# Performance work log

Measured on AMD Instinct MI355X. Metric: run time of the kernel, lower is better.

The kernel has to match this reference:

```python
import jax, jax.numpy as jnp
import numpy as np
from jax.scipy.linalg import expm
jax.config.update("jax_enable_x64", True)

HBAR = 0.6582119569
CM2EV = 0.00012398419
N6A, N10A = 4, 4
DT = 1.0
KDC = dict(E_S1=3.995, E_S2=4.9183, om6a=596.0 * CM2EV, om10a=919.0 * CM2EV,
           kap6a_S1=-0.0964, kap6a_S2=0.1193, lam=0.1825, gamma=-0.018)


def _build():
    cd = np.complex128

    def ladder(n):
        a = np.zeros((n, n), dtype=cd)
        for k in range(1, n):
            a[k - 1, k] = np.sqrt(float(k))
        adag = a.conj().T
        return (a + adag) / np.sqrt(2.0), adag @ a, np.eye(n, dtype=cd)

    Q6a1, N6a1, I6a = ladder(N6A)
    Q10a1, N10a1, I10a = ladder(N10A)
    Nel, Dvib = 3, N6A * N10A
    Ivib = np.eye(Dvib, dtype=cd)
    Iel = np.eye(Nel, dtype=cd)
    lift = lambda op: np.kron(Iel, op)
    Q6a = lift(np.kron(Q6a1, I10a))
    Q10a = lift(np.kron(I6a, Q10a1))
    N6a = lift(np.kron(N6a1, I10a))
    N10a = lift(np.kron(I6a, N10a1))
    P = []
    for k in range(Nel):
        ek = np.zeros(Nel, dtype=cd); ek[k] = 1.0
        P.append(np.kron(np.outer(ek, ek), Ivib))
    e1 = np.zeros(Nel, dtype=cd); e1[1] = 1.0
    e2 = np.zeros(Nel, dtype=cd); e2[2] = 1.0
    Poff = np.kron(np.outer(e1, e2) + np.outer(e2, e1), Ivib)
    Lj = np.kron(np.outer(e1, e2), Ivib)  # |S1><S2| lift
    D = Nel * Dvib
    I = np.eye(D, dtype=cd)
    p = KDC
    H = (p['E_S1'] * P[1] + p['E_S2'] * P[2] + p['om6a'] * N6a + p['om10a'] * N10a
         + p['kap6a_S1'] * P[1] @ Q6a + p['kap6a_S2'] * P[2] @ Q6a
         + p['lam'] * Poff @ Q10a + p['gamma'] * Poff @ (Q10a @ Q10a))
    # Coherent part -i(I kron H - H^T* kron I); dissipator at unit rate (scaled by g later)
    Lc = -1j * (np.kron(I, H) - np.kron(H.conj().T, I))
    LdL = Lj.conj().T @ Lj
    Ld0 = (np.kron(Lj.conj(), Lj) - 0.5 * np.kron(I, LdL)
           - 0.5 * np.kron(LdL.conj().T, I))
    psi = np.zeros(D, dtype=cd); psi[2 * N6A * N10A] = 1.0
    rho0 = np.outer(psi, psi.conj()).reshape(-1)
    trP = np.stack([P[k].T.reshape(-1) for k in range(3)])  # [3, D^2]
    return Lc, Ld0, rho0, trP

_LC, _LD0, _RHO0, _TRP = _build()


def setup_inputs() -> dict:
    return {"log_g": jnp.asarray(np.log(1.0 / 40.0), dtype=jnp.float32),
            "n_steps": 1000}


def reference(log_g, n_steps):
    Lc = jnp.asarray(_LC)
    Ld0 = jnp.asarray(_LD0)
    rho0 = jnp.asarray(_RHO0)
    trP = jnp.asarray(_TRP)
    g = jnp.exp(log_g).astype(jnp.float64)
    Lsup = Lc + g * Ld0                      # [D^2, D^2] complex128
    U = expm(Lsup * (DT / HBAR))             # one-step propagator

    def step(rho, _):
        pops = jnp.real(trP @ rho)           # tr(P_k rho), k=0..2
        return U @ rho, pops

    _, ps = jax.lax.scan(step, rho0, None, length=int(n_steps))  # [n_steps, 3]
    return (ps[:, 0].astype(jnp.float32),
            ps[:, 1].astype(jnp.float32),
            ps[:, 2].astype(jnp.float32))
```

## Files before the change

### kernel.cpp

```cpp
#include <hip/hip_runtime.h>
#include <math.h>


#define DS 1024
#define MATD ((size_t)DS * DS * sizeof(double))
#define PA 66

typedef double v4d __attribute__((ext_vector_type(4)));

__device__ inline double Qel(int i, int j) {
    if (i == j + 1) return sqrt((double)i) * 0.70710678118654752440;
    if (j == i + 1) return sqrt((double)j) * 0.70710678118654752440;
    return 0.0;
}

__device__ inline void fill_H(double* Hs, int tid) {
    const double CM2EV = 0.00012398419;
    const double E_S1 = 3.995, E_S2 = 4.9183;
    const double om6a = 596.0 * CM2EV, om10a = 919.0 * CM2EV;
    const double kapA = -0.0964, kapB = 0.1193, lam = 0.1825, gam = -0.018;
    for (int h = tid; h < 1024; h += 256) {
        int r = h >> 5, c = h & 31;
        int e = r >> 4, v6 = (r >> 2) & 3, v10 = r & 3;
        int e2 = c >> 4, w6 = (c >> 2) & 3, w10 = c & 3;
        double val = 0.0;
        if (r == c) val += (e ? E_S2 : E_S1) + om6a * v6 + om10a * v10;
        if (e == e2 && v10 == w10) val += (e ? kapB : kapA) * Qel(v6, w6);
        if (e != e2 && v6 == w6) {
            double q2 = 0.0;
            #pragma unroll
            for (int m = 0; m < 4; ++m) q2 += Qel(v10, m) * Qel(m, w10);
            val += lam * Qel(v10, w10) + gam * q2;
        }
        Hs[h] = val;
    }
}

__global__ __launch_bounds__(256)
void build_G10(const float* __restrict__ logg, double* __restrict__ X,
               double* __restrict__ Y, double* __restrict__ Z)
{
    int tid = threadIdx.x;
    if (blockIdx.x >= 4096) {
        int idx = (blockIdx.x - 4096) * 256 + tid;
        if (idx < 64 * 1024) {
            int r = idx >> 10, i = idx & 1023;
            double v = 0.0;
            if (r < 2 && i % 33 == 0) {
                int a = i / 33;
                if ((a < 16) == (r == 0)) v = 1.0;
            }
            Y[idx] = v;
        } else if (idx < 64 * 1024 + 1024) {
            int i = idx - 64 * 1024;
            Z[i] = (i == 528) ? 1.0 : 0.0;
        }
        return;
    }
    __shared__ double Hs[1024];
    fill_H(Hs, tid);
    __syncthreads();
    double g = exp((double)logg[0]);
    const double sc = ((1.0 / 0.6582119569) / 16.0) / 10.0;
    int idx = blockIdx.x * 256 + tid;
    int r = idx >> 10, c = idx & 1023;
    int i = r >> 5, j = r & 31;
    int k = c >> 5, l = c & 31;
    double t = 0.0;
    if (k <= l) {
        if (i <= j) {
            if (i < 16 && j < 16) {
                int p = i + 16, q = j + 16;
                if ((p == k && q == l) || (p == l && q == k)) t += g;
            }
            if (i == k && j == l) t -= 0.5 * g * ((i >= 16) + (j >= 16));
        } else {
            if (j == l) t += Hs[i * 32 + k];
            if (k != l && j == k) t += Hs[i * 32 + l];
            if (i == k) t -= Hs[l * 32 + j];
            if (k != l && i == l) t -= Hs[k * 32 + j];
        }
    } else {
        if (i <= j) {
            double ha = 0.0;
            if (j == l) ha += Hs[i * 32 + k];
            if (j == k) ha -= Hs[i * 32 + l];
            if (i == k) ha -= Hs[l * 32 + j];
            if (i == l) ha += Hs[k * 32 + j];
            t -= ha;
        } else {
            if (i < 16 && j < 16 && (i + 16 == k) && (j + 16 == l)) t += g;
            if (i == k && j == l) t -= 0.5 * g * ((i >= 16) + (j >= 16));
        }
    }
    X[idx] = t * sc + ((r == c) ? 1.0 : 0.0);
}

__global__ __launch_bounds__(256)
void apply_T(const float* __restrict__ logg, const double* __restrict__ M,
             double* __restrict__ O, double invk)
{
    __shared__ double Hs[1024];
    __shared__ int    qlist[112];
    __shared__ double wl[4][112];
    __shared__ int    counts[4];
    __shared__ int    Kshared;
    const int tid = threadIdx.x;
    fill_H(Hs, tid);
    __syncthreads();
    const double g = exp((double)logg[0]);
    const double sck = ((1.0 / 0.6582119569) / 16.0) * invk;

    const int a = blockIdx.x >> 4, b = blockIdx.x & 15;
    const int i0 = a << 1, j0 = b << 1;
    const int wv = tid >> 6, lane = tid & 63;
    const int m = lane & 31;

    bool valid = false; int q = 0;
    double w0 = 0.0, w1 = 0.0, w2 = 0.0, w3 = 0.0;

    if (a != b) {
        if (lane < 32) {
            const bool fam2 = (wv >= 2);
            const int sel = wv & 1;
            if (!fam2) {
                const int js = j0 + sel;
                double cA = Hs[i0 * 32 + m];
                double cB = Hs[(i0 + 1) * 32 + m];
                if (a < b) {
                    if ((cA != 0.0 || cB != 0.0) && m != js) {
                        valid = true;
                        q = (m > js) ? m * 32 + js : js * 32 + m;
                        double sA = (m > js) ? -cA : cA;
                        double sB = (m > js) ? -cB : cB;
                        if (sel == 0) { w0 = sA; w2 = sB; }
                        else          { w1 = sA; w3 = sB; }
                    }
                } else {
                    if (cA != 0.0 || cB != 0.0) {
                        valid = true;
                        q = (m < js) ? m * 32 + js : js * 32 + m;
                        if (sel == 0) { w0 = cA; w2 = cB; }
                        else          { w1 = cA; w3 = cB; }
                    }
                }
            } else {
                const int is = i0 + sel;
                double c0 = Hs[m * 32 + j0];
                double c1 = Hs[m * 32 + j0 + 1];
                if (a < b) {
                    if ((c0 != 0.0 || c1 != 0.0) && m != is) {
                        valid = true;
                        q = (is > m) ? is * 32 + m : m * 32 + is;
                        double s0 = (is > m) ? c0 : -c0;
                        double s1 = (is > m) ? c1 : -c1;
                        if (sel == 0) { w0 = s0; w1 = s1; }
                        else          { w2 = s0; w3 = s1; }
                    }
                } else {
                    if (c0 != 0.0 || c1 != 0.0) {
                        valid = true;
                        q = (m < is) ? m * 32 + is : is * 32 + m;
                        if (sel == 0) { w0 = -c0; w1 = -c1; }
                        else          { w2 = -c0; w3 = -c1; }
                    }
                }
            }
        }
    } else {
        const int ia = i0 + (wv >> 1), ja = j0 + (wv & 1);
        const bool up = (ia <= ja);
        double wr = 0.0;
        if (lane < 32) {
            double c = Hs[ia * 32 + m];
            if (up) {
                if (c != 0.0 && m != ja) {
                    valid = true;
                    q = (m > ja) ? m * 32 + ja : ja * 32 + m;
                    wr = (m > ja) ? -c : c;
                }
            } else {
                if (c != 0.0) {
                    valid = true;
                    q = (m < ja) ? m * 32 + ja : ja * 32 + m;
                    wr = c;
                }
            }
        } else {
            double c = Hs[m * 32 + ja];
            if (up) {
                if (c != 0.0 && m != ia) {
                    valid = true;
                    q = (ia > m) ? ia * 32 + m : m * 32 + ia;
                    wr = (ia > m) ? c : -c;
                }
            } else {
                if (c != 0.0) {
                    valid = true;
                    q = (m < ia) ? m * 32 + ia : ia * 32 + m;
                    wr = -c;
                }
            }
        }
        if (wv == 0) w0 = wr; else if (wv == 1) w1 = wr;
        else if (wv == 2) w2 = wr; else w3 = wr;
    }

    unsigned long long mask = __ballot(valid);
    if (lane == 0) counts[wv] = __popcll(mask);
    __syncthreads();
    int base = 0;
    for (int t = 0; t < wv; ++t) base += counts[t];
    if (valid) {
        int slot = base + __popcll(mask & ((1ull << lane) - 1ull));
        qlist[slot] = q;
        wl[0][slot] = w0; wl[1][slot] = w1; wl[2][slot] = w2; wl[3][slot] = w3;
    }
    __syncthreads();
    if (tid == 0) {
        int K = counts[0] + counts[1] + counts[2] + counts[3];
        const int cnt = (a >= 8) + (b >= 8);
        if (a < 8 && b < 8) {
            #pragma unroll
            for (int r = 0; r < 4; ++r) {
                int ia = i0 + (r >> 1), ja = j0 + (r & 1);
                qlist[K] = (ia + 16) * 32 + (ja + 16);
                wl[0][K] = 0.0; wl[1][K] = 0.0; wl[2][K] = 0.0; wl[3][K] = 0.0;
                wl[r][K] = g; ++K;
            }
        }
        if (cnt > 0) {
            double wd = -0.5 * g * (double)cnt;
            #pragma unroll
            for (int r = 0; r < 4; ++r) {
                int ia = i0 + (r >> 1), ja = j0 + (r & 1);
                qlist[K] = ia * 32 + ja;
                wl[0][K] = 0.0; wl[1][K] = 0.0; wl[2][K] = 0.0; wl[3][K] = 0.0;
                wl[r][K] = wd; ++K;
            }
        }
        while (K & 1) {
            qlist[K] = 0;
            wl[0][K] = 0.0; wl[1][K] = 0.0; wl[2][K] = 0.0; wl[3][K] = 0.0;
            ++K;
        }
        Kshared = K;
    }
    __syncthreads();
    const int K = Kshared;

    double acc[4][4];
    #pragma unroll
    for (int r = 0; r < 4; ++r)
        #pragma unroll
        for (int u = 0; u < 4; ++u) acc[r][u] = 0.0;

    const double2* Mp = (const double2*)M;
    const int e2 = tid << 1;
    for (int k = 0; k < K; k += 2) {
        #pragma unroll
        for (int u = 0; u < 2; ++u) {
            int qq = qlist[k + u];
            double W0 = wl[0][k + u], W1 = wl[1][k + u];
            double W2 = wl[2][k + u], W3 = wl[3][k + u];
            double2 v0 = Mp[(size_t)qq * (DS / 2) + e2];
            double2 v1 = Mp[(size_t)qq * (DS / 2) + e2 + 1];
            acc[0][0] += W0 * v0.x; acc[0][1] += W0 * v0.y;
            acc[0][2] += W0 * v1.x; acc[0][3] += W0 * v1.y;
            acc[1][0] += W1 * v0.x; acc[1][1] += W1 * v0.y;
            acc[1][2] += W1 * v1.x; acc[1][3] += W1 * v1.y;
            acc[2][0] += W2 * v0.x; acc[2][1] += W2 * v0.y;
            acc[2][2] += W2 * v1.x; acc[2][3] += W2 * v1.y;
            acc[3][0] += W3 * v0.x; acc[3][1] += W3 * v0.y;
            acc[3][2] += W3 * v1.x; acc[3][3] += W3 * v1.y;
        }
    }

    const int c0 = tid << 2;
    #pragma unroll
    for (int r = 0; r < 4; ++r) {
        int pr = (i0 + (r >> 1)) * 32 + (j0 + (r & 1));
        size_t bse = (size_t)pr * DS + c0;
        O[bse + 0] = sck * acc[r][0] + ((pr == c0)     ? 1.0 : 0.0);
        O[bse + 1] = sck * acc[r][1] + ((pr == c0 + 1) ? 1.0 : 0.0);
        O[bse + 2] = sck * acc[r][2] + ((pr == c0 + 2) ? 1.0 : 0.0);
        O[bse + 3] = sck * acc[r][3] + ((pr == c0 + 3) ? 1.0 : 0.0);
    }
}

__global__ __launch_bounds__(1024, 1)
void dgemm(const double* __restrict__ A, const double* __restrict__ B,
           double* __restrict__ D)
{
    __shared__ double As[2][64 * PA];
    __shared__ double Bs[2][64 * PA];
    const int tid = threadIdx.x;
    const int bm = blockIdx.x << 6, bn = blockIdx.y << 6;
    const int w = tid >> 6, lane = tid & 63;
    const int lr = lane & 15, lk = lane >> 4;
    const int p = w & 3, kg = w >> 2;
    const int wr = (p >> 1) << 5, wc = (p & 1) << 5;

    v4d acc[2][2];
    #pragma unroll
    for (int si = 0; si < 2; ++si)
        #pragma unroll
        for (int sj = 0; sj < 2; ++sj) acc[si][sj] = (v4d){0., 0., 0., 0.};

    const int ra = tid >> 4;
    const int cs = (tid & 15) << 2;
    const double* gA = A + (size_t)(bm + ra) * DS + cs;
    const double* gB = B + (size_t)ra * DS + bn + cs;
    double va[4], vb[4];
    #pragma unroll
    for (int u = 0; u < 4; ++u) { va[u] = gA[u]; vb[u] = gB[u]; }
    #pragma unroll
    for (int u = 0; u < 4; ++u) {
        As[0][ra * PA + cs + u] = va[u];
        Bs[0][ra * PA + cs + u] = vb[u];
    }
    #pragma unroll
    for (int u = 0; u < 4; ++u) {
        va[u] = gA[64 + u];
        vb[u] = gB[(size_t)64 * DS + u];
    }
    __syncthreads();

    #pragma unroll 2
    for (int kt = 0; kt < DS; kt += 64) {
        const int pb = (kt >> 6) & 1;
        const bool more  = (kt + 64) < DS;
        const bool more2 = (kt + 128) < DS;
        const int k0 = (kg << 4) + lk;
        double A00 = As[pb][(wr + lr) * PA + k0];
        double A10 = As[pb][(wr + 16 + lr) * PA + k0];
        double B00 = Bs[pb][k0 * PA + wc + lr];
        double B10 = Bs[pb][k0 * PA + wc + 16 + lr];
        double A01 = As[pb][(wr + lr) * PA + k0 + 4];
        double A11 = As[pb][(wr + 16 + lr) * PA + k0 + 4];
        double B01 = Bs[pb][(k0 + 4) * PA + wc + lr];
        double B11 = Bs[pb][(k0 + 4) * PA + wc + 16 + lr];
        acc[0][0] = __builtin_amdgcn_mfma_f64_16x16x4f64(A00, B00, acc[0][0], 0, 0, 0);
        acc[0][1] = __builtin_amdgcn_mfma_f64_16x16x4f64(A00, B10, acc[0][1], 0, 0, 0);
        acc[1][0] = __builtin_amdgcn_mfma_f64_16x16x4f64(A10, B00, acc[1][0], 0, 0, 0);
        acc[1][1] = __builtin_amdgcn_mfma_f64_16x16x4f64(A10, B10, acc[1][1], 0, 0, 0);
        acc[0][0] = __builtin_amdgcn_mfma_f64_16x16x4f64(A01, B01, acc[0][0], 0, 0, 0);
        acc[0][1] = __builtin_amdgcn_mfma_f64_16x16x4f64(A01, B11, acc[0][1], 0, 0, 0);
        acc[1][0] = __builtin_amdgcn_mfma_f64_16x16x4f64(A11, B01, acc[1][0], 0, 0, 0);
        acc[1][1] = __builtin_amdgcn_mfma_f64_16x16x4f64(A11, B11, acc[1][1], 0, 0, 0);
        if (more) {
            #pragma unroll
            for (int u = 0; u < 4; ++u) {
                As[pb ^ 1][ra * PA + cs + u] = va[u];
                Bs[pb ^ 1][ra * PA + cs + u] = vb[u];
            }
        }
        if (more2) {
            #pragma unroll
            for (int u = 0; u < 4; ++u) {
                va[u] = gA[kt + 128 + u];
                vb[u] = gB[(size_t)(kt + 128) * DS + u];
            }
        }
        double A02 = As[pb][(wr + lr) * PA + k0 + 8];
        double A12 = As[pb][(wr + 16 + lr) * PA + k0 + 8];
        double B02 = Bs[pb][(k0 + 8) * PA + wc + lr];
        double B12 = Bs[pb][(k0 + 8) * PA + wc + 16 + lr];
        double A03 = As[pb][(wr + lr) * PA + k0 + 12];
        double A13 = As[pb][(wr + 16 + lr) * PA + k0 + 12];
        double B03 = Bs[pb][(k0 + 12) * PA + wc + lr];
        double B13 = Bs[pb][(k0 + 12) * PA + wc + 16 + lr];
        acc[0][0] = __builtin_amdgcn_mfma_f64_16x16x4f64(A02, B02, acc[0][0], 0, 0, 0);
        acc[0][1] = __builtin_amdgcn_mfma_f64_16x16x4f64(A02, B12, acc[0][1], 0, 0, 0);
        acc[1][0] = __builtin_amdgcn_mfma_f64_16x16x4f64(A12, B02, acc[1][0], 0, 0, 0);
        acc[1][1] = __builtin_amdgcn_mfma_f64_16x16x4f64(A12, B12, acc[1][1], 0, 0, 0);
        acc[0][0] = __builtin_amdgcn_mfma_f64_16x16x4f64(A03, B03, acc[0][0], 0, 0, 0);
        acc[0][1] = __builtin_amdgcn_mfma_f64_16x16x4f64(A03, B13, acc[0][1], 0, 0, 0);
        acc[1][0] = __builtin_amdgcn_mfma_f64_16x16x4f64(A13, B03, acc[1][0], 0, 0, 0);
        acc[1][1] = __builtin_amdgcn_mfma_f64_16x16x4f64(A13, B13, acc[1][1], 0, 0, 0);
        __syncthreads();
    }

    double* red = &As[0][0];
    if (kg == 3) {
        #pragma unroll
        for (int si = 0; si < 2; ++si)
            #pragma unroll
            for (int sj = 0; sj < 2; ++sj)
                #pragma unroll
                for (int r = 0; r < 4; ++r)
                    red[(wr + si * 16 + lk + 4 * r) * 64 + wc + sj * 16 + lr]
                        = acc[si][sj][r];
    }
    __syncthreads();
    if (kg == 2) {
        #pragma unroll
        for (int si = 0; si < 2; ++si)
            #pragma unroll
            for (int sj = 0; sj < 2; ++sj)
                #pragma unroll
                for (int r = 0; r < 4; ++r)
                    red[(wr + si * 16 + lk + 4 * r) * 64 + wc + sj * 16 + lr]
                        += acc[si][sj][r];
    }
    __syncthreads();
    if (kg == 1) {
        #pragma unroll
        for (int si = 0; si < 2; ++si)
            #pragma unroll
            for (int sj = 0; sj < 2; ++sj)
                #pragma unroll
                for (int r = 0; r < 4; ++r)
                    red[(wr + si * 16 + lk + 4 * r) * 64 + wc + sj * 16 + lr]
                        += acc[si][sj][r];
    }
    __syncthreads();
    if (kg == 0) {
        #pragma unroll
        for (int si = 0; si < 2; ++si)
            #pragma unroll
            for (int sj = 0; sj < 2; ++sj) {
                int col = bn + wc + sj * 16 + lr;
                #pragma unroll
                for (int r = 0; r < 4; ++r) {
                    int row = bm + wr + si * 16 + lk + 4 * r;
                    D[(size_t)row * DS + col] = acc[si][sj][r]
                        + red[(wr + si * 16 + lk + 4 * r) * 64 + wc + sj * 16 + lr];
                }
            }
    }
}

__global__ __launch_bounds__(256)
void ypart(const double* __restrict__ P, const double* __restrict__ Y,
           double* __restrict__ scratch, int SR)
{
    __shared__ double Yld[32 * 64];
    __shared__ double red[32 * 64];
    const int tid = threadIdx.x;
    const int cc = tid & 63, kw = tid >> 6;
    const int col = (blockIdx.x << 6) + cc;
    const int r0 = blockIdx.z << 5;

    double acc[32];
    #pragma unroll
    for (int r = 0; r < 32; ++r) acc[r] = 0.0;

    for (int kt = 0; kt < 4; ++kt) {
        const int kb = ((blockIdx.y << 2) + kt) << 6;
        __syncthreads();
        for (int idx = tid; idx < 32 * 64; idx += 256) {
            int r = idx >> 6, kk = idx & 63;
            Yld[idx] = Y[(size_t)(r0 + r) * DS + kb + kk];
        }
        __syncthreads();
        #pragma unroll
        for (int kk = 0; kk < 16; ++kk) {
            int kl = (kw << 4) + kk;
            double pv = P[(size_t)(kb + kl) * DS + col];
            #pragma unroll
            for (int r = 0; r < 32; ++r)
                acc[r] += Yld[(r << 6) + kl] * pv;
        }
    }

    __syncthreads();
    if (kw == 3) {
        #pragma unroll
        for (int r = 0; r < 32; ++r) red[(r << 6) + cc] = acc[r];
    }
    __syncthreads();
    if (kw == 2) {
        #pragma unroll
        for (int r = 0; r < 32; ++r) red[(r << 6) + cc] += acc[r];
    }
    __syncthreads();
    if (kw == 1) {
        #pragma unroll
        for (int r = 0; r < 32; ++r) red[(r << 6) + cc] += acc[r];
    }
    __syncthreads();
    if (kw == 0) {
        #pragma unroll
        for (int r = 0; r < 32; ++r) red[(r << 6) + cc] += acc[r];
    }
    __syncthreads();
    for (int idx = tid; idx < 32 * 64; idx += 256) {
        int r = idx >> 6, c2 = idx & 63;
        scratch[((size_t)blockIdx.y * SR + r0 + r) * DS + (blockIdx.x << 6) + c2]
            = red[idx];
    }
}

__global__ __launch_bounds__(256)
void yreduce(const double* __restrict__ scratch, double* __restrict__ Y,
             int M, int SR)
{
    int idx = blockIdx.x * 256 + threadIdx.x;
    int r = idx >> 10, c = idx & 1023;
    double s = 0.0;
    #pragma unroll
    for (int q = 0; q < 4; ++q)
        s += scratch[((size_t)q * SR + r) * DS + c];
    Y[(size_t)(M + r) * DS + c] = s;
}

__global__ __launch_bounds__(256)
void zstep(const double* __restrict__ V, const double* __restrict__ Zin,
           double* __restrict__ Zout)
{
    int row = blockIdx.x * 4 + (threadIdx.x >> 6);
    int lane = threadIdx.x & 63;
    const double2* r_ = (const double2*)(V + (size_t)row * DS);
    const double2* z_ = (const double2*)Zin;
    double s = 0.0;
    #pragma unroll
    for (int k = 0; k < 8; ++k) {
        double2 a = r_[(k << 6) + lane];
        double2 b = z_[(k << 6) + lane];
        s += a.x * b.x + a.y * b.y;
    }
    #pragma unroll
    for (int off = 32; off; off >>= 1) s += __shfl_down(s, off);
    if (lane == 0) Zout[row] = s;
}

__global__ __launch_bounds__(128)
void final_pops(const double* __restrict__ Y, const double* __restrict__ Z,
                float* __restrict__ out, int n)
{
    int t = blockIdx.x;
    int k = threadIdx.x >> 6, lane = threadIdx.x & 63;
    int a = t & 31, j = t >> 5;
    const double* y = Y + (size_t)(2 * a + k) * 1024;
    const double* z = Z + (size_t)j * 1024;
    double s = 0.0;
    for (int i = lane; i < 1024; i += 64) s += y[i] * z[i];
    #pragma unroll
    for (int off = 32; off; off >>= 1) s += __shfl_down(s, off);
    if (lane == 0) {
        out[(size_t)(k + 1) * n + t] = (float)s;
        if (k == 0) out[t] = 0.0f;
    }
}

static inline void ydouble2(const double* P, double* Y, double* scr, int M,
                            hipStream_t stream)
{
    int gz = (M + 31) / 32; if (gz < 1) gz = 1;
    int SR = gz * 32;
    ypart<<<dim3(16, 4, gz), 256, 0, stream>>>(P, Y, scr, SR);
    yreduce<<<SR * 4, 256, 0, stream>>>(scr, Y, M, SR);
}

extern "C" void kernel_launch(void* const* d_in, const int* in_sizes, int n_in,
                              void* d_out, int out_size, void* d_ws, size_t ws_size,
                              hipStream_t stream)
{
    const float* logg = (const float*)d_in[0];
    float* out = (float*)d_out;
    const int n = out_size / 3;
    (void)in_sizes; (void)n_in; (void)ws_size;

    char* ws = (char*)d_ws;
    double* b0 = (double*)(ws + 0 * MATD);
    double* b1 = (double*)(ws + 1 * MATD);
    double* b2 = (double*)(ws + 2 * MATD);
    double* scr = (double*)(ws + 3 * MATD);
    double* Y  = (double*)(ws + 5 * MATD);
    double* Z  = Y + 64 * 1024;

    dim3 g2(16, 16);

    build_G10<<<4096 + 260, 256, 0, stream>>>(logg, b0, Y, Z);
    double* src = b0; double* dst = b1;
    for (int k = 9; k >= 1; --k) {
        apply_T<<<256, 256, 0, stream>>>(logg, src, dst, 1.0 / (double)k);
        double* t = src; src = dst; dst = t;
    }

    dgemm<<<g2, 1024, 0, stream>>>(b1, b1, b0);
    dgemm<<<g2, 1024, 0, stream>>>(b0, b0, b2);
    dgemm<<<g2, 1024, 0, stream>>>(b2, b2, b1);
    dgemm<<<g2, 1024, 0, stream>>>(b1, b1, b0);
    ydouble2(b0, Y, scr, 2, stream);
    dgemm<<<g2, 1024, 0, stream>>>(b0, b0, b1);
    ydouble2(b1, Y, scr, 4, stream);
    dgemm<<<g2, 1024, 0, stream>>>(b1, b1, b2);
    ydouble2(b2, Y, scr, 8, stream);
    dgemm<<<g2, 1024, 0, stream>>>(b2, b2, b1);
    ydouble2(b1, Y, scr, 16, stream);
    dgemm<<<g2, 1024, 0, stream>>>(b1, b1, b2);
    ydouble2(b2, Y, scr, 32, stream);
    dgemm<<<g2, 1024, 0, stream>>>(b2, b2, b1);

    for (int j = 1; j < 32; ++j)
        zstep<<<256, 256, 0, stream>>>(b1, Z + (size_t)(j - 1) * 1024,
                                       Z + (size_t)j * 1024);

    final_pops<<<n, 128, 0, stream>>>(Y, Z, out, n);
}
```

Measured before the change: 763.1 us.

## Split apply_T and ypart work across more blocks for higher parallelism

apply_T now launches 1024 blocks, each handling a quarter of the columns with one element per thread, and uses a swizzled block index so the same row group is spread across XCDs. Its inner loop is unrolled by 8, with the nonzero list padded to a multiple of 8. ypart is split over 16 K-chunks instead of 4 looping ones, and yreduce now sums 16 partials. The aim is to fill the GPU better in these small kernels, at the cost of redundant per-block H setup and more scratch traffic in the reduction.

```diff
diff --git a/kernel.cpp b/kernel.cpp
--- a/kernel.cpp
+++ b/kernel.cpp
@@ -101,8 +101,8 @@
              double* __restrict__ O, double invk)
 {
     __shared__ double Hs[1024];
-    __shared__ int    qlist[112];
-    __shared__ double wl[4][112];
+    __shared__ int    qlist[120];
+    __shared__ double wl[4][120];
     __shared__ int    counts[4];
     __shared__ int    Kshared;
     const int tid = threadIdx.x;
@@ -111,7 +111,9 @@
     const double g = exp((double)logg[0]);
     const double sck = ((1.0 / 0.6582119569) / 16.0) * invk;
 
-    const int a = blockIdx.x >> 4, b = blockIdx.x & 15;
+    const int sw = ((blockIdx.x & 7) << 7) | (blockIdx.x >> 3);
+    const int grp = sw >> 2, q4 = sw & 3;
+    const int a = grp >> 4, b = grp & 15;
     const int i0 = a << 1, j0 = b << 1;
     const int wv = tid >> 6, lane = tid & 63;
     const int m = lane & 31;
@@ -239,7 +241,7 @@
                 wl[r][K] = wd; ++K;
             }
         }
-        while (K & 1) {
+        while (K & 7) {
             qlist[K] = 0;
             wl[0][K] = 0.0; wl[1][K] = 0.0; wl[2][K] = 0.0; wl[3][K] = 0.0;
             ++K;
@@ -249,42 +251,25 @@
     __syncthreads();
     const int K = Kshared;
 
-    double acc[4][4];
-    #pragma unroll
-    for (int r = 0; r < 4; ++r)
-        #pragma unroll
-        for (int u = 0; u < 4; ++u) acc[r][u] = 0.0;
-
-    const double2* Mp = (const double2*)M;
-    const int e2 = tid << 1;
-    for (int k = 0; k < K; k += 2) {
-        #pragma unroll
-        for (int u = 0; u < 2; ++u) {
+    const int col = (q4 << 8) + tid;
+    double a0 = 0.0, a1 = 0.0, a2 = 0.0, a3 = 0.0;
+    for (int k = 0; k < K; k += 8) {
+        #pragma unroll
+        for (int u = 0; u < 8; ++u) {
             int qq = qlist[k + u];
-            double W0 = wl[0][k + u], W1 = wl[1][k + u];
-            double W2 = wl[2][k + u], W3 = wl[3][k + u];
-            double2 v0 = Mp[(size_t)qq * (DS / 2) + e2];
-            double2 v1 = Mp[(size_t)qq * (DS / 2) + e2 + 1];
-            acc[0][0] += W0 * v0.x; acc[0][1] += W0 * v0.y;
-            acc[0][2] += W0 * v1.x; acc[0][3] += W0 * v1.y;
-            acc[1][0] += W1 * v0.x; acc[1][1] += W1 * v0.y;
-            acc[1][2] += W1 * v1.x; acc[1][3] += W1 * v1.y;
-            acc[2][0] += W2 * v0.x; acc[2][1] += W2 * v0.y;
-            acc[2][2] += W2 * v1.x; acc[2][3] += W2 * v1.y;
-            acc[3][0] += W3 * v0.x; acc[3][1] += W3 * v0.y;
-            acc[3][2] += W3 * v1.x; acc[3][3] += W3 * v1.y;
-        }
-    }
-
-    const int c0 = tid << 2;
+            double v = M[(size_t)qq * DS + col];
+            a0 += wl[0][k + u] * v;
+            a1 += wl[1][k + u] * v;
+            a2 += wl[2][k + u] * v;
+            a3 += wl[3][k + u] * v;
+        }
+    }
+
+    double accs[4] = {a0, a1, a2, a3};
     #pragma unroll
     for (int r = 0; r < 4; ++r) {
         int pr = (i0 + (r >> 1)) * 32 + (j0 + (r & 1));
-        size_t bse = (size_t)pr * DS + c0;
-        O[bse + 0] = sck * acc[r][0] + ((pr == c0)     ? 1.0 : 0.0);
-        O[bse + 1] = sck * acc[r][1] + ((pr == c0 + 1) ? 1.0 : 0.0);
-        O[bse + 2] = sck * acc[r][2] + ((pr == c0 + 2) ? 1.0 : 0.0);
-        O[bse + 3] = sck * acc[r][3] + ((pr == c0 + 3) ? 1.0 : 0.0);
+        O[(size_t)pr * DS + col] = sck * accs[r] + ((pr == col) ? 1.0 : 0.0);
     }
 }
 
@@ -440,28 +425,26 @@
     const int tid = threadIdx.x;
     const int cc = tid & 63, kw = tid >> 6;
     const int col = (blockIdx.x << 6) + cc;
+    const int kb = blockIdx.y << 6;
     const int r0 = blockIdx.z << 5;
 
+    for (int idx = tid; idx < 32 * 64; idx += 256) {
+        int r = idx >> 6, kk = idx & 63;
+        Yld[idx] = Y[(size_t)(r0 + r) * DS + kb + kk];
+    }
+    __syncthreads();
+
     double acc[32];
     #pragma unroll
     for (int r = 0; r < 32; ++r) acc[r] = 0.0;
 
-    for (int kt = 0; kt < 4; ++kt) {
-        const int kb = ((blockIdx.y << 2) + kt) << 6;
-        __syncthreads();
-        for (int idx = tid; idx < 32 * 64; idx += 256) {
-            int r = idx >> 6, kk = idx & 63;
-            Yld[idx] = Y[(size_t)(r0 + r) * DS + kb + kk];
-        }
-        __syncthreads();
-        #pragma unroll
-        for (int kk = 0; kk < 16; ++kk) {
-            int kl = (kw << 4) + kk;
-            double pv = P[(size_t)(kb + kl) * DS + col];
-            #pragma unroll
-            for (int r = 0; r < 32; ++r)
-                acc[r] += Yld[(r << 6) + kl] * pv;
-        }
+    #pragma unroll
+    for (int kk = 0; kk < 16; ++kk) {
+        int kl = (kw << 4) + kk;
+        double pv = P[(size_t)(kb + kl) * DS + col];
+        #pragma unroll
+        for (int r = 0; r < 32; ++r)
+            acc[r] += Yld[(r << 6) + kl] * pv;
     }
 
     __syncthreads();
@@ -500,7 +483,7 @@
     int r = idx >> 10, c = idx & 1023;
     double s = 0.0;
     #pragma unroll
-    for (int q = 0; q < 4; ++q)
+    for (int q = 0; q < 16; ++q)
         s += scratch[((size_t)q * SR + r) * DS + c];
     Y[(size_t)(M + r) * DS + c] = s;
 }
@@ -549,7 +532,7 @@
 {
     int gz = (M + 31) / 32; if (gz < 1) gz = 1;
     int SR = gz * 32;
-    ypart<<<dim3(16, 4, gz), 256, 0, stream>>>(P, Y, scr, SR);
+    ypart<<<dim3(16, 16, gz), 256, 0, stream>>>(P, Y, scr, SR);
     yreduce<<<SR * 4, 256, 0, stream>>>(scr, Y, M, SR);
 }
 
@@ -575,7 +558,7 @@
     build_G10<<<4096 + 260, 256, 0, stream>>>(logg, b0, Y, Z);
     double* src = b0; double* dst = b1;
     for (int k = 9; k >= 1; --k) {
-        apply_T<<<256, 256, 0, stream>>>(logg, src, dst, 1.0 / (double)k);
+        apply_T<<<1024, 256, 0, stream>>>(logg, src, dst, 1.0 / (double)k);
         double* t = src; src = dst; dst = t;
     }
 
```

Measured after the change: 644.2 us (median of 2 runs). 15.6% less time.
